# Kernel tuning notes

Measured on AMD Instinct MI355X. Metric: run time of the kernel, lower is better.

## Reference

```python
import jax, jax.numpy as jnp
import numpy as np

N = 50000
E = 600000
IN_DIM = 2000
HID = 64
OUT_DIM = 25
HEADS = 4
NHEAD = 4
NLAYERS = 2
FF = 2048
EPS = 1e-5


def gat_conv(x, W, a_src, a_dst, b, src, dst, heads, out_dim):
    n = x.shape[0]
    h = (x @ W).reshape(n, heads, out_dim)
    # per-node attention logits
    al_src = jnp.sum(h * a_src[None], axis=-1)  # [N,H]
    al_dst = jnp.sum(h * a_dst[None], axis=-1)  # [N,H]
    e = jax.nn.leaky_relu(al_src[src] + al_dst[dst], negative_slope=0.2)  # [E,H]
    # segment softmax over destination nodes (every node has a self-loop)
    m = jax.ops.segment_max(e, dst, num_segments=n)
    ex = jnp.exp(e - m[dst])
    s = jax.ops.segment_sum(ex, dst, num_segments=n)
    alpha = ex / (s[dst] + 1e-16)  # [E,H]
    msg = h[src] * alpha[..., None]  # [E,H,out]
    out = jax.ops.segment_sum(msg, dst, num_segments=n)  # [N,H,out]
    return out.reshape(n, heads * out_dim) + b


def layer_norm(x, g, b):
    mu = jnp.mean(x, axis=-1, keepdims=True)
    var = jnp.mean(jnp.square(x - mu), axis=-1, keepdims=True)
    return (x - mu) * jax.lax.rsqrt(var + EPS) * g + b


def encoder_layer(x, Wq, Wk, Wv, bq, bk, bv, Wo, bo, g1, b1, Wf1, bf1, Wf2, bf2, g2, b2):
    # seq_len = 1: each node is its own length-1 sequence -> softmax weights are 1
    n, d = x.shape
    dh = d // NHEAD
    q = (x @ Wq + bq).reshape(n, NHEAD, dh)
    k = (x @ Wk + bk).reshape(n, NHEAD, dh)
    v = (x @ Wv + bv).reshape(n, NHEAD, dh)
    s = jnp.sum(q * k, axis=-1, keepdims=True) / jnp.sqrt(jnp.float32(dh))  # [N,H,1]
    a = jax.nn.softmax(s, axis=-1)  # all ones (length-1 softmax)
    attn = (a * v).reshape(n, d) @ Wo + bo
    x = layer_norm(x + attn, g1, b1)
    ff = jax.nn.relu(x @ Wf1 + bf1) @ Wf2 + bf2
    return layer_norm(x + ff, g2, b2)


def setup_inputs() -> dict:
    key = jax.random.key(0)
    ks = jax.random.split(key, 40)
    sc = 0.05
    inp = {}
    inp["x"] = jax.random.normal(ks[0], (N, IN_DIM), dtype=jnp.float32)
    inp["edge_src"] = jax.random.randint(ks[1], (E,), 0, N, dtype=jnp.int32)
    inp["edge_dst"] = jax.random.randint(ks[2], (E,), 0, N, dtype=jnp.int32)
    # GAT layer 1: in -> hidden, heads=4
    inp["W1"] = jax.random.normal(ks[3], (IN_DIM, HEADS * HID), dtype=jnp.float32) * sc
    inp["a_src1"] = jax.random.normal(ks[4], (HEADS, HID), dtype=jnp.float32) * sc
    inp["a_dst1"] = jax.random.normal(ks[5], (HEADS, HID), dtype=jnp.float32) * sc
    inp["b1"] = jnp.zeros((HEADS * HID,), dtype=jnp.float32)
    # GAT layer 2: hidden*heads -> hidden, heads=1
    inp["W2"] = jax.random.normal(ks[6], (HEADS * HID, HID), dtype=jnp.float32) * sc
    inp["a_src2"] = jax.random.normal(ks[7], (1, HID), dtype=jnp.float32) * sc
    inp["a_dst2"] = jax.random.normal(ks[8], (1, HID), dtype=jnp.float32) * sc
    inp["b2"] = jnp.zeros((HID,), dtype=jnp.float32)
    # Transformer fusion params, stacked over layers
    def pl(k, shape):
        return jax.random.normal(k, shape, dtype=jnp.float32) * sc
    inp["t_Wq"] = pl(ks[9], (NLAYERS, HID, HID))
    inp["t_Wk"] = pl(ks[10], (NLAYERS, HID, HID))
    inp["t_Wv"] = pl(ks[11], (NLAYERS, HID, HID))
    inp["t_bq"] = jnp.zeros((NLAYERS, HID), dtype=jnp.float32)
    inp["t_bk"] = jnp.zeros((NLAYERS, HID), dtype=jnp.float32)
    inp["t_bv"] = jnp.zeros((NLAYERS, HID), dtype=jnp.float32)
    inp["t_Wo"] = pl(ks[12], (NLAYERS, HID, HID))
    inp["t_bo"] = jnp.zeros((NLAYERS, HID), dtype=jnp.float32)
    inp["t_ln1g"] = jnp.ones((NLAYERS, HID), dtype=jnp.float32)
    inp["t_ln1b"] = jnp.zeros((NLAYERS, HID), dtype=jnp.float32)
    inp["t_Wff1"] = pl(ks[13], (NLAYERS, HID, FF))
    inp["t_bff1"] = jnp.zeros((NLAYERS, FF), dtype=jnp.float32)
    inp["t_Wff2"] = pl(ks[14], (NLAYERS, FF, HID))
    inp["t_bff2"] = jnp.zeros((NLAYERS, HID), dtype=jnp.float32)
    inp["t_ln2g"] = jnp.ones((NLAYERS, HID), dtype=jnp.float32)
    inp["t_ln2b"] = jnp.zeros((NLAYERS, HID), dtype=jnp.float32)
    # GAT ADT head: hidden -> out, heads=1
    inp["W3"] = pl(ks[15], (HID, OUT_DIM))
    inp["a_src3"] = pl(ks[16], (1, OUT_DIM))
    inp["a_dst3"] = pl(ks[17], (1, OUT_DIM))
    inp["b3"] = jnp.zeros((OUT_DIM,), dtype=jnp.float32)
    return inp


def reference(x, edge_src, edge_dst, W1, a_src1, a_dst1, b1, W2, a_src2, a_dst2, b2,
              t_Wq, t_Wk, t_Wv, t_bq, t_bk, t_bv, t_Wo, t_bo, t_ln1g, t_ln1b,
              t_Wff1, t_bff1, t_Wff2, t_bff2, t_ln2g, t_ln2b,
              W3, a_src3, a_dst3, b3):
    # add self-loops (PyG GATConv default add_self_loops=True)
    loops = jnp.arange(N, dtype=edge_src.dtype)
    src = jnp.concatenate([edge_src, loops])
    dst = jnp.concatenate([edge_dst, loops])

    h = gat_conv(x, W1, a_src1, a_dst1, b1, src, dst, HEADS, HID)
    h = jax.nn.elu(h)
    rna = gat_conv(h, W2, a_src2, a_dst2, b2, src, dst, 1, HID)
    rna = jax.nn.elu(rna)

    fused = rna
    for l in range(NLAYERS):
        fused = encoder_layer(fused, t_Wq[l], t_Wk[l], t_Wv[l], t_bq[l], t_bk[l], t_bv[l],
                              t_Wo[l], t_bo[l], t_ln1g[l], t_ln1b[l],
                              t_Wff1[l], t_bff1[l], t_Wff2[l], t_bff2[l],
                              t_ln2g[l], t_ln2b[l])

    adt_pred = gat_conv(fused, W3, a_src3, a_dst3, b3, src, dst, 1, OUT_DIM)
    return (adt_pred, fused)
```

## Files before the change

kernel.cpp:

```cpp
#include <hip/hip_runtime.h>
#include <math.h>

#define N_NODES 50000
#define IN_DIMC 2000
#define FF_DIM 2048
#define EPSV 1e-5f
#define SCAN_B 1024

typedef __attribute__((ext_vector_type(8))) short sh8;
typedef __attribute__((ext_vector_type(4))) short sh4;
typedef __attribute__((ext_vector_type(4))) float f32x4;

__device__ __forceinline__ void splitf(float f, unsigned short& h, unsigned short& l) {
    unsigned u = __float_as_uint(f);
    h = (unsigned short)(u >> 16);
    float fh = __uint_as_float(u & 0xFFFF0000u);
    l = (unsigned short)(__float_as_uint(f - fh) >> 16);
}

__device__ __forceinline__ void split8(f32x4 a0, f32x4 a1, sh8& hh, sh8& ll) {
    float f[8] = {a0[0], a0[1], a0[2], a0[3], a1[0], a1[1], a1[2], a1[3]};
    sh8 h, l;
#pragma unroll
    for (int j = 0; j < 8; j++) {
        unsigned u = __float_as_uint(f[j]);
        h[j] = (short)(u >> 16);
        float fhi = __uint_as_float(u & 0xFFFF0000u);
        l[j] = (short)(__float_as_uint(f[j] - fhi) >> 16);
    }
    hh = h; ll = l;
}

__device__ __forceinline__ void gload_lds16(const float* g, float* l) {
    __builtin_amdgcn_global_load_lds(
        (const __attribute__((address_space(1))) unsigned int*)g,
        (__attribute__((address_space(3))) unsigned int*)l, 16, 0, 0);
}

__global__ void k_zero_i32(int* p, int n) {
    int i = blockIdx.x * blockDim.x + threadIdx.x;
    if (i < n) p[i] = 0;
}

__global__ void k_hist(const int* __restrict__ dst, int* __restrict__ deg, int E, int n) {
    int i = blockIdx.x * blockDim.x + threadIdx.x;
    if (i < E + n) {
        int d = (i < E) ? dst[i] : (i - E);
        atomicAdd(&deg[d], 1);
    }
}

__global__ __launch_bounds__(1024) void k_scan1(const int* __restrict__ deg, int* __restrict__ rstart,
                                                int* __restrict__ part, int n) {
    __shared__ int lds[SCAN_B];
    int t = threadIdx.x;
    int base = blockIdx.x * SCAN_B;
    int v = (base + t < n) ? deg[base + t] : 0;
    lds[t] = v;
    __syncthreads();
    for (int o = 1; o < SCAN_B; o <<= 1) {
        int add = (t >= o) ? lds[t - o] : 0;
        __syncthreads();
        lds[t] += add;
        __syncthreads();
    }
    if (base + t < n) rstart[base + t] = lds[t] - v;
    if (t == SCAN_B - 1) part[blockIdx.x] = lds[t];
}

__global__ void k_scan2(int* part, int nb) {
    if (threadIdx.x == 0 && blockIdx.x == 0) {
        int s = 0;
        for (int i = 0; i < nb; i++) { int v = part[i]; part[i] = s; s += v; }
    }
}

__global__ void k_scan3(int* rstart, const int* __restrict__ part, int n) {
    int i = blockIdx.x * blockDim.x + threadIdx.x;
    if (i < n) rstart[i] += part[i / SCAN_B];
}

__global__ void k_scatter(const int* __restrict__ src, const int* __restrict__ dst,
                          const int* __restrict__ rstart, int* __restrict__ cursor,
                          int* __restrict__ csr_src, int E, int n) {
    int i = blockIdx.x * blockDim.x + threadIdx.x;
    if (i < E + n) {
        int s, d;
        if (i < E) { s = src[i]; d = dst[i]; } else { s = i - E; d = s; }
        int pos = rstart[d] + atomicAdd(&cursor[d], 1);
        csr_src[pos] = s;
    }
}

__global__ void k_wsplit_pad(const float* __restrict__ W, short* __restrict__ oh,
                             short* __restrict__ ol, int K, int N, int Kpad, int Npad) {
    int i = blockIdx.x * blockDim.x + threadIdx.x;
    if (i < Kpad * Npad) {
        int c = i / Kpad, k = i - c * Kpad;
        float v = (c < N && k < K) ? W[(size_t)k * N + c] : 0.f;
        unsigned short h, l;
        splitf(v, h, l);
        oh[i] = (short)h; ol[i] = (short)l;
    }
}

__global__ void k_wsplit(const float* __restrict__ W, short* __restrict__ oh,
                         short* __restrict__ ol, int K, int N) {
    int i = blockIdx.x * blockDim.x + threadIdx.x;
    if (i < K * N) {
        int k = i / N, c = i - k * N;
        unsigned short h, l;
        splitf(W[i], h, l);
        oh[(size_t)c * K + k] = (short)h;
        ol[(size_t)c * K + k] = (short)l;
    }
}

__global__ void k_wcomb(const float* __restrict__ Wv, const float* __restrict__ bv,
                        const float* __restrict__ Wo, const float* __restrict__ bo,
                        short* __restrict__ och, short* __restrict__ ocl, float* __restrict__ bc) {
    int i = blockIdx.x * blockDim.x + threadIdx.x;
    if (i < 4096) {
        int cc = i & 63, kk = i >> 6;
        float s = 0.f;
        for (int j = 0; j < 64; j++) s += Wv[kk * 64 + j] * Wo[j * 64 + cc];
        unsigned short h, l;
        splitf(s, h, l);
        och[cc * 64 + kk] = (short)h;
        ocl[cc * 64 + kk] = (short)l;
        if (kk == 0) {
            float t = bo[cc];
            for (int j = 0; j < 64; j++) t += bv[j] * Wo[j * 64 + cc];
            bc[cc] = t;
        }
    }
}

template<int NF>
__global__ __launch_bounds__(256, 2) void k_gemm_x(const float* __restrict__ A,
                                                   const short* __restrict__ Bth,
                                                   const short* __restrict__ Btl,
                                                   const float* __restrict__ bias,
                                                   float* __restrict__ C,
                                                   int M, int N, int K, int Kpad) {
    constexpr int BN = NF * 32;
    __shared__ float Afs[128 * 64];
    __shared__ short Bhs[BN * 64];
    __shared__ short Bls[BN * 64];
    int tid = threadIdx.x;
    int wave = tid >> 6, lane = tid & 63;
    int wm = wave & 1, wn = wave >> 1;
    int l15 = lane & 15, l4 = lane >> 4;
    long m0 = (long)blockIdx.x * 128;
    int n0 = blockIdx.y * BN;
    int chunks = K >> 2;
    int cmax = chunks - 1;
    int ktiles = (chunks + 15) >> 4;
    f32x4 acc[4][NF] = {};
    int Sl = wave * 512 + lane;
    for (int kt = 0; kt < ktiles; kt++) {
        int c0 = kt << 4;
#pragma unroll
        for (int i = 0; i < 8; i++) {
            int S = Sl + i * 64;
            int row = S >> 4, slot = S & 15;
            long srcrow = m0 + row; if (srcrow > (long)M - 1) srcrow = M - 1;
            int ch = c0 + (slot ^ (row & 7)); if (ch > cmax) ch = cmax;
            gload_lds16(A + (size_t)srcrow * K + (size_t)ch * 4,
                        &Afs[(wave * 512 + i * 64) * 4]);
        }
#pragma unroll
        for (int p = 0; p < NF; p++) {
            int u = tid + p * 256;
            int col = u >> 3, k8 = u & 7;
            size_t src = (size_t)(n0 + col) * Kpad + (size_t)kt * 64 + k8 * 8;
            sh8 bh = *(const sh8*)&Bth[src];
            sh8 bl = *(const sh8*)&Btl[src];
            int doff = col * 64 + ((k8 ^ (col & 7)) << 3);
            *(sh8*)&Bhs[doff] = bh;
            *(sh8*)&Bls[doff] = bl;
        }
        __syncthreads();
#pragma unroll
        for (int kf = 0; kf < 2; kf++) {
            sh8 ah[4], al[4];
#pragma unroll
            for (int mf = 0; mf < 4; mf++) {
                int row = wm * 64 + mf * 16 + l15;
                int s0 = kf * 8 + l4 * 2;
                f32x4 a0 = *(const f32x4*)&Afs[row * 64 + ((s0 ^ (row & 7)) << 2)];
                f32x4 a1 = *(const f32x4*)&Afs[row * 64 + (((s0 + 1) ^ (row & 7)) << 2)];
                split8(a0, a1, ah[mf], al[mf]);
            }
#pragma unroll
            for (int nf = 0; nf < NF; nf++) {
                int col = wn * (NF * 16) + nf * 16 + l15;
                int k8 = kf * 4 + l4;
                int boff = col * 64 + ((k8 ^ (col & 7)) << 3);
                sh8 bh = *(const sh8*)&Bhs[boff];
                sh8 bl = *(const sh8*)&Bls[boff];
#pragma unroll
                for (int mf = 0; mf < 4; mf++) {
                    f32x4 c = acc[mf][nf];
                    c = __builtin_amdgcn_mfma_f32_16x16x32_bf16(ah[mf], bh, c, 0, 0, 0);
                    c = __builtin_amdgcn_mfma_f32_16x16x32_bf16(ah[mf], bl, c, 0, 0, 0);
                    c = __builtin_amdgcn_mfma_f32_16x16x32_bf16(al[mf], bh, c, 0, 0, 0);
                    acc[mf][nf] = c;
                }
            }
        }
        __syncthreads();
    }
#pragma unroll
    for (int mf = 0; mf < 4; mf++)
#pragma unroll
        for (int r = 0; r < 4; r++) {
            long gm = m0 + wm * 64 + mf * 16 + l4 * 4 + r;
            if (gm >= M) continue;
#pragma unroll
            for (int nf = 0; nf < NF; nf++) {
                int gc = n0 + wn * (NF * 16) + nf * 16 + l15;
                if (gc < N) C[gm * (size_t)N + gc] = acc[mf][nf][r] + (bias ? bias[gc] : 0.f);
            }
        }
}

__global__ __launch_bounds__(256, 2) void k_ff_mfma(const float* __restrict__ x,
                                                    const short* __restrict__ W1h, const short* __restrict__ W1l,
                                                    const float* __restrict__ bf1,
                                                    const short* __restrict__ W2h, const short* __restrict__ W2l,
                                                    const float* __restrict__ bf2,
                                                    float* __restrict__ out, int n) {
    __shared__ short lds[36864];
    short* Hh = lds;
    short* Hl = lds + 9216;
    short* w1h = lds + 18432;
    short* w1l = lds + 23040;
    short* w2h = lds + 27648;
    short* w2l = lds + 32256;
    int tid = threadIdx.x;
    int wave = tid >> 6, lane = tid & 63;
    int wm = wave & 1, wn = wave >> 1;
    int l15 = lane & 15, l4 = lane >> 4;
    long row0 = (long)blockIdx.x * 128;
#pragma unroll
    for (int p = 0; p < 8; p++) {
        int f4 = tid + p * 256;
        int row = f4 >> 4, kq = f4 & 15;
        long gr = row0 + row;
        float4 a = {0.f, 0.f, 0.f, 0.f};
        if (gr < n) a = *(const float4*)&x[gr * 64 + kq * 4];
        unsigned short h0, h1, h2, h3, l0, l1, l2, l3;
        splitf(a.x, h0, l0); splitf(a.y, h1, l1);
        splitf(a.z, h2, l2); splitf(a.w, h3, l3);
        sh4 hv = {(short)h0, (short)h1, (short)h2, (short)h3};
        sh4 lv = {(short)l0, (short)l1, (short)l2, (short)l3};
        *(sh4*)&Hh[row * 72 + kq * 4] = hv;
        *(sh4*)&Hl[row * 72 + kq * 4] = lv;
    }
    __syncthreads();
    sh8 xh[4][2], xl[4][2];
#pragma unroll
    for (int mf = 0; mf < 4; mf++)
#pragma unroll
        for (int kf = 0; kf < 2; kf++) {
            int off = (wm * 64 + mf * 16 + l15) * 72 + kf * 32 + l4 * 8;
            xh[mf][kf] = *(const sh8*)&Hh[off];
            xl[mf][kf] = *(const sh8*)&Hl[off];
        }
    f32x4 acc2[4][2] = {};
    for (int j0 = 0; j0 < FF_DIM; j0 += 64) {
#pragma unroll
        for (int p = 0; p < 2; p++) {
            int u = tid + p * 256;
            int cj = u >> 3, kq8 = u & 7;
            *(sh8*)&w1h[cj * 72 + kq8 * 8] = *(const sh8*)&W1h[(size_t)(j0 + cj) * 64 + kq8 * 8];
            *(sh8*)&w1l[cj * 72 + kq8 * 8] = *(const sh8*)&W1l[(size_t)(j0 + cj) * 64 + kq8 * 8];
            *(sh8*)&w2h[cj * 72 + kq8 * 8] = *(const sh8*)&W2h[(size_t)cj * FF_DIM + j0 + kq8 * 8];
            *(sh8*)&w2l[cj * 72 + kq8 * 8] = *(const sh8*)&W2l[(size_t)cj * FF_DIM + j0 + kq8 * 8];
        }
        __syncthreads();
        f32x4 hacc[4][2] = {};
#pragma unroll
        for (int kf = 0; kf < 2; kf++) {
            sh8 bh[2], bl[2];
#pragma unroll
            for (int nf = 0; nf < 2; nf++) {
                int off = (wn * 32 + nf * 16 + l15) * 72 + kf * 32 + l4 * 8;
                bh[nf] = *(const sh8*)&w1h[off];
                bl[nf] = *(const sh8*)&w1l[off];
            }
#pragma unroll
            for (int mf = 0; mf < 4; mf++)
#pragma unroll
                for (int nf = 0; nf < 2; nf++) {
                    f32x4 c = hacc[mf][nf];
                    c = __builtin_amdgcn_mfma_f32_16x16x32_bf16(xh[mf][kf], bh[nf], c, 0, 0, 0);
                    c = __builtin_amdgcn_mfma_f32_16x16x32_bf16(xh[mf][kf], bl[nf], c, 0, 0, 0);
                    c = __builtin_amdgcn_mfma_f32_16x16x32_bf16(xl[mf][kf], bh[nf], c, 0, 0, 0);
                    hacc[mf][nf] = c;
                }
        }
#pragma unroll
        for (int mf = 0; mf < 4; mf++)
#pragma unroll
            for (int nf = 0; nf < 2; nf++) {
                int col = wn * 32 + nf * 16 + l15;
                float b1v = bf1[j0 + col];
#pragma unroll
                for (int r = 0; r < 4; r++) {
                    int row = wm * 64 + mf * 16 + l4 * 4 + r;
                    float v = fmaxf(hacc[mf][nf][r] + b1v, 0.f);
                    unsigned short h, l;
                    splitf(v, h, l);
                    Hh[row * 72 + col] = (short)h;
                    Hl[row * 72 + col] = (short)l;
                }
            }
        __syncthreads();
#pragma unroll
        for (int kf = 0; kf < 2; kf++) {
            sh8 ah[4], alv[4], bh[2], bl[2];
#pragma unroll
            for (int mf = 0; mf < 4; mf++) {
                int off = (wm * 64 + mf * 16 + l15) * 72 + kf * 32 + l4 * 8;
                ah[mf] = *(const sh8*)&Hh[off];
                alv[mf] = *(const sh8*)&Hl[off];
            }
#pragma unroll
            for (int nf = 0; nf < 2; nf++) {
                int off = (wn * 32 + nf * 16 + l15) * 72 + kf * 32 + l4 * 8;
                bh[nf] = *(const sh8*)&w2h[off];
                bl[nf] = *(const sh8*)&w2l[off];
            }
#pragma unroll
            for (int mf = 0; mf < 4; mf++)
#pragma unroll
                for (int nf = 0; nf < 2; nf++) {
                    f32x4 c = acc2[mf][nf];
                    c = __builtin_amdgcn_mfma_f32_16x16x32_bf16(ah[mf], bh[nf], c, 0, 0, 0);
                    c = __builtin_amdgcn_mfma_f32_16x16x32_bf16(ah[mf], bl[nf], c, 0, 0, 0);
                    c = __builtin_amdgcn_mfma_f32_16x16x32_bf16(alv[mf], bh[nf], c, 0, 0, 0);
                    acc2[mf][nf] = c;
                }
        }
        __syncthreads();
    }
#pragma unroll
    for (int mf = 0; mf < 4; mf++)
#pragma unroll
        for (int r = 0; r < 4; r++) {
            long gr = row0 + wm * 64 + mf * 16 + l4 * 4 + r;
            if (gr >= n) continue;
#pragma unroll
            for (int nf = 0; nf < 2; nf++) {
                int gc = wn * 32 + nf * 16 + l15;
                out[gr * 64 + gc] = acc2[mf][nf][r] + bf2[gc];
            }
        }
}

template<int H, int D>
__global__ void k_al(const float* __restrict__ h, const float* __restrict__ a_src,
                     const float* __restrict__ a_dst, float* __restrict__ als,
                     float* __restrict__ ald, int n) {
    long w = ((long)blockIdx.x * blockDim.x + threadIdx.x) >> 6;
    int lane = threadIdx.x & 63;
    long nn = w / H;
    int hh = (int)(w % H);
    if (nn >= n) return;
    float v = 0.f, u = 0.f;
    if (lane < D) {
        float hv = h[nn * (H * D) + hh * D + lane];
        v = hv * a_src[hh * D + lane];
        u = hv * a_dst[hh * D + lane];
    }
#pragma unroll
    for (int o = 32; o > 0; o >>= 1) {
        v += __shfl_xor(v, o, 64);
        u += __shfl_xor(u, o, 64);
    }
    if (lane == 0) { als[nn * H + hh] = v; ald[nn * H + hh] = u; }
}

template<int H, int D, bool DO_ELU>
__global__ __launch_bounds__(256) void k_gat_agg_w(const float* __restrict__ h,
                                                   const float* __restrict__ als,
                                                   const float* __restrict__ ald,
                                                   const float* __restrict__ bias,
                                                   const int* __restrict__ rstart,
                                                   const int* __restrict__ deg,
                                                   const int* __restrict__ csr_src,
                                                   float* __restrict__ out, int n) {
    int wid = (int)(((long)blockIdx.x * blockDim.x + threadIdx.x) >> 6);
    int lane = threadIdx.x & 63;
    if (wid >= n) return;
    int beg = rstart[wid], cnt = deg[wid];
    float aldv = 0.f;
    if (lane < H) aldv = ald[wid * H + lane];
    float wsum = 0.f;
    float acc[H];
#pragma unroll
    for (int i = 0; i < H; i++) acc[i] = 0.f;
    for (int e = 0; e < cnt; e++) {
        int s = csr_src[beg + e];
        float w = 0.f;
        if (lane < H) {
            float lg = als[s * H + lane] + aldv;
            lg = (lg > 0.f) ? lg : 0.2f * lg;
            w = __expf(lg);
            wsum += w;
        }
#pragma unroll
        for (int hh = 0; hh < H; hh++) {
            float wv = __shfl(w, hh, 64);
            float hv = (lane < D) ? h[(size_t)s * (H * D) + hh * D + lane] : 0.f;
            acc[hh] += wv * hv;
        }
    }
#pragma unroll
    for (int hh = 0; hh < H; hh++) {
        float ws = __shfl(wsum, hh, 64);
        if (lane < D) {
            float v = acc[hh] / (ws + 1e-16f) + bias[hh * D + lane];
            if (DO_ELU) v = (v > 0.f) ? v : expm1f(v);
            out[(size_t)wid * (H * D) + hh * D + lane] = v;
        }
    }
}

__global__ void k_ln(const float* __restrict__ x, const float* __restrict__ y,
                     const float* __restrict__ g, const float* __restrict__ b,
                     float* __restrict__ out, int n) {
    long w = ((long)blockIdx.x * blockDim.x + threadIdx.x) >> 6;
    int lane = threadIdx.x & 63;
    if (w >= n) return;
    float v = x[w * 64 + lane] + y[w * 64 + lane];
    float s = v;
#pragma unroll
    for (int o = 32; o > 0; o >>= 1) s += __shfl_xor(s, o, 64);
    float mu = s * (1.f / 64.f);
    float dv = v - mu;
    float q = dv * dv;
#pragma unroll
    for (int o = 32; o > 0; o >>= 1) q += __shfl_xor(q, o, 64);
    float var = q * (1.f / 64.f);
    out[w * 64 + lane] = dv * rsqrtf(var + EPSV) * g[lane] + b[lane];
}

extern "C" void kernel_launch(void* const* d_in, const int* in_sizes, int n_in,
                              void* d_out, int out_size, void* d_ws, size_t ws_size,
                              hipStream_t stream) {
    const float* x = (const float*)d_in[0];
    const int* esrc = (const int*)d_in[1];
    const int* edst = (const int*)d_in[2];
    const float* W1 = (const float*)d_in[3];
    const float* as1 = (const float*)d_in[4];
    const float* ad1 = (const float*)d_in[5];
    const float* b1 = (const float*)d_in[6];
    const float* W2 = (const float*)d_in[7];
    const float* as2 = (const float*)d_in[8];
    const float* ad2 = (const float*)d_in[9];
    const float* b2 = (const float*)d_in[10];
    const float* tWv = (const float*)d_in[13];
    const float* tbv = (const float*)d_in[16];
    const float* tWo = (const float*)d_in[17];
    const float* tbo = (const float*)d_in[18];
    const float* tg1 = (const float*)d_in[19];
    const float* tb1 = (const float*)d_in[20];
    const float* tWf1 = (const float*)d_in[21];
    const float* tbf1 = (const float*)d_in[22];
    const float* tWf2 = (const float*)d_in[23];
    const float* tbf2 = (const float*)d_in[24];
    const float* tg2 = (const float*)d_in[25];
    const float* tb2 = (const float*)d_in[26];
    const float* W3 = (const float*)d_in[27];
    const float* as3 = (const float*)d_in[28];
    const float* ad3 = (const float*)d_in[29];
    const float* b3 = (const float*)d_in[30];

    const int n = N_NODES;
    const int E = in_sizes[1];
    const int ET = E + n;

    float* fw = (float*)d_ws;
    float* h1 = fw;
    float* agg1 = fw + 12800000;
    float* bufA = fw + 25600000;
    float* bufB = fw + 28800000;
    float* bufC = fw + 32000000;
    float* bufD = fw + 35200000;
    float* als = fw + 38400000;
    float* ald = fw + 38600000;
    float* bc = fw + 38800000;
    int* deg = (int*)(fw + 38800064);
    int* rstart = deg + 50016;
    int* cursor = rstart + 50016;
    int* part = cursor + 50016;
    int* csr = part + 64;
    short* sbase = (short*)(csr + 700000);
    short* w1th = sbase;
    short* w1tl = w1th + 524288;
    short* w2th = w1tl + 524288;
    short* w2tl = w2th + 16384;
    short* w3th = w2tl + 16384;
    short* w3tl = w3th + 4096;
    short* wcth = w3tl + 4096;
    short* wctl = wcth + 4096;
    const size_t WFS = 131072;
    short* wf1h = wctl + 4096;
    short* wf1l = wf1h + 2 * WFS;
    short* wf2h = wf1l + 2 * WFS;
    short* wf2l = wf2h + 2 * WFS;
    float* h3 = h1;

    float* outAdt = (float*)d_out;
    float* outFused = outAdt + (size_t)n * 25;

    k_zero_i32<<<(150048 + 255) / 256, 256, 0, stream>>>(deg, 150048);
    k_hist<<<(ET + 255) / 256, 256, 0, stream>>>(edst, deg, E, n);
    int nsb = (n + SCAN_B - 1) / SCAN_B;
    k_scan1<<<nsb, SCAN_B, 0, stream>>>(deg, rstart, part, n);
    k_scan2<<<1, 64, 0, stream>>>(part, nsb);
    k_scan3<<<(n + 255) / 256, 256, 0, stream>>>(rstart, part, n);
    k_scatter<<<(ET + 255) / 256, 256, 0, stream>>>(esrc, edst, rstart, cursor, csr, E, n);

    k_wsplit_pad<<<(524288 + 255) / 256, 256, 0, stream>>>(W1, w1th, w1tl, IN_DIMC, 256, 2048, 256);
    k_wsplit_pad<<<(16384 + 255) / 256, 256, 0, stream>>>(W2, w2th, w2tl, 256, 64, 256, 64);
    k_wsplit_pad<<<(4096 + 255) / 256, 256, 0, stream>>>(W3, w3th, w3tl, 64, 25, 64, 64);
    for (int l = 0; l < 2; l++) {
        k_wsplit<<<(131072 + 255) / 256, 256, 0, stream>>>(tWf1 + (size_t)l * 64 * FF_DIM,
                                                           wf1h + l * WFS, wf1l + l * WFS, 64, FF_DIM);
        k_wsplit<<<(131072 + 255) / 256, 256, 0, stream>>>(tWf2 + (size_t)l * FF_DIM * 64,
                                                           wf2h + l * WFS, wf2l + l * WFS, FF_DIM, 64);
    }

    k_gemm_x<4><<<dim3((n + 127) / 128, 2), 256, 0, stream>>>(x, w1th, w1tl, nullptr, h1, n, 256, IN_DIMC, 2048);
    k_al<4, 64><<<n, 256, 0, stream>>>(h1, as1, ad1, als, ald, n);
    k_gat_agg_w<4, 64, true><<<(n + 3) / 4, 256, 0, stream>>>(h1, als, ald, b1, rstart, deg, csr, agg1, n);

    k_gemm_x<2><<<dim3((n + 127) / 128, 1), 256, 0, stream>>>(agg1, w2th, w2tl, nullptr, bufA, n, 64, 256, 256);
    k_al<1, 64><<<(n + 3) / 4, 256, 0, stream>>>(bufA, as2, ad2, als, ald, n);
    k_gat_agg_w<1, 64, true><<<(n + 3) / 4, 256, 0, stream>>>(bufA, als, ald, b2, rstart, deg, csr, bufB, n);

    float* xin = bufB;
    for (int l = 0; l < 2; l++) {
        k_wcomb<<<16, 256, 0, stream>>>(tWv + (size_t)l * 4096, tbv + (size_t)l * 64,
                                        tWo + (size_t)l * 4096, tbo + (size_t)l * 64,
                                        wcth, wctl, bc);
        k_gemm_x<2><<<dim3((n + 127) / 128, 1), 256, 0, stream>>>(xin, wcth, wctl, bc, bufD, n, 64, 64, 64);
        k_ln<<<(n + 3) / 4, 256, 0, stream>>>(xin, bufD, tg1 + (size_t)l * 64, tb1 + (size_t)l * 64, bufA, n);
        k_ff_mfma<<<(n + 127) / 128, 256, 0, stream>>>(bufA, wf1h + l * WFS, wf1l + l * WFS,
                                                       tbf1 + (size_t)l * FF_DIM,
                                                       wf2h + l * WFS, wf2l + l * WFS,
                                                       tbf2 + (size_t)l * 64, bufC, n);
        float* xout = (l == 1) ? outFused : bufB;
        k_ln<<<(n + 3) / 4, 256, 0, stream>>>(bufA, bufC, tg2 + (size_t)l * 64, tb2 + (size_t)l * 64, xout, n);
        xin = xout;
    }

    k_gemm_x<2><<<dim3((n + 127) / 128, 1), 256, 0, stream>>>(outFused, w3th, w3tl, nullptr, h3, n, 25, 64, 64);
    k_al<1, 25><<<(n + 3) / 4, 256, 0, stream>>>(h3, as3, ad3, als, ald, n);
    k_gat_agg_w<1, 25, false><<<(n + 3) / 4, 256, 0, stream>>>(h3, als, ald, b3, rstart, deg, csr, outAdt, n);
}
```

Measured before the change: 1.484 ms.

## Double-buffer GEMM tiles via direct LDS loads and vectorize GAT aggregation kernels

The split-bf16 GEMM now uses two LDS buffers with a K-tile of 32, and loads B high/low halves directly into LDS with global_load_lds, so the next tile is fetched while MFMAs run on the current one. The generic GAT aggregation kernel is replaced by three specialized ones. The 4-head version uses float4 loads and processes two edges per iteration. The single-head versions split the wave across several edges at once and reduce with shuffles. The aim is to hide load latency in the large first GEMM and to cut idle lanes and scalar gathers in the bandwidth-bound edge aggregation. The cost is more synchronization per K step and extra register pressure.

```diff
diff --git a/kernel.cpp b/kernel.cpp
--- a/kernel.cpp
+++ b/kernel.cpp
@@ -31,7 +31,7 @@
     hh = h; ll = l;
 }
 
-__device__ __forceinline__ void gload_lds16(const float* g, float* l) {
+__device__ __forceinline__ void gload_lds16(const void* g, void* l) {
     __builtin_amdgcn_global_load_lds(
         (const __attribute__((address_space(1))) unsigned int*)g,
         (__attribute__((address_space(3))) unsigned int*)l, 16, 0, 0);
@@ -137,79 +137,80 @@
 }
 
 template<int NF>
-__global__ __launch_bounds__(256, 2) void k_gemm_x(const float* __restrict__ A,
+__global__ __launch_bounds__(256, 2) void k_gemm_p(const float* __restrict__ A,
                                                    const short* __restrict__ Bth,
                                                    const short* __restrict__ Btl,
                                                    const float* __restrict__ bias,
                                                    float* __restrict__ C,
                                                    int M, int N, int K, int Kpad) {
     constexpr int BN = NF * 32;
-    __shared__ float Afs[128 * 64];
-    __shared__ short Bhs[BN * 64];
-    __shared__ short Bls[BN * 64];
+    constexpr int NB = BN / 32;
+    __shared__ float Afs[2][128 * 32];
+    __shared__ short Bs[2][BN * 64];
     int tid = threadIdx.x;
     int wave = tid >> 6, lane = tid & 63;
     int wm = wave & 1, wn = wave >> 1;
     int l15 = lane & 15, l4 = lane >> 4;
     long m0 = (long)blockIdx.x * 128;
     int n0 = blockIdx.y * BN;
-    int chunks = K >> 2;
-    int cmax = chunks - 1;
-    int ktiles = (chunks + 15) >> 4;
+    int cmax = (K >> 2) - 1;
+    int ktiles = (K + 31) >> 5;
     f32x4 acc[4][NF] = {};
-    int Sl = wave * 512 + lane;
-    for (int kt = 0; kt < ktiles; kt++) {
-        int c0 = kt << 4;
-#pragma unroll
-        for (int i = 0; i < 8; i++) {
-            int S = Sl + i * 64;
-            int row = S >> 4, slot = S & 15;
+
+    auto stage = [&](int kt, int b) {
+        int c0 = kt << 3;
+#pragma unroll
+        for (int i = 0; i < 4; i++) {
+            int S = (wave * 4 + i) * 64 + lane;
+            int row = S >> 3, slot = S & 7;
             long srcrow = m0 + row; if (srcrow > (long)M - 1) srcrow = M - 1;
             int ch = c0 + (slot ^ (row & 7)); if (ch > cmax) ch = cmax;
             gload_lds16(A + (size_t)srcrow * K + (size_t)ch * 4,
-                        &Afs[(wave * 512 + i * 64) * 4]);
-        }
-#pragma unroll
-        for (int p = 0; p < NF; p++) {
-            int u = tid + p * 256;
-            int col = u >> 3, k8 = u & 7;
-            size_t src = (size_t)(n0 + col) * Kpad + (size_t)kt * 64 + k8 * 8;
-            sh8 bh = *(const sh8*)&Bth[src];
-            sh8 bl = *(const sh8*)&Btl[src];
-            int doff = col * 64 + ((k8 ^ (col & 7)) << 3);
-            *(sh8*)&Bhs[doff] = bh;
-            *(sh8*)&Bls[doff] = bl;
+                        &Afs[b][(wave * 4 + i) * 256]);
+        }
+#pragma unroll
+        for (int i = 0; i < NB; i++) {
+            int S = (wave * NB + i) * 64 + lane;
+            int col = S >> 3, slot = S & 7;
+            int c = slot ^ (col & 7);
+            const short* src = (c < 4)
+                ? Bth + (size_t)(n0 + col) * Kpad + kt * 32 + c * 8
+                : Btl + (size_t)(n0 + col) * Kpad + kt * 32 + (c - 4) * 8;
+            gload_lds16(src, &Bs[b][(wave * NB + i) * 512]);
+        }
+    };
+
+    stage(0, 0);
+    __syncthreads();
+    int b = 0;
+    for (int kt = 0; kt < ktiles; kt++) {
+        if (kt + 1 < ktiles) stage(kt + 1, b ^ 1);
+        sh8 ah[4], al[4];
+#pragma unroll
+        for (int mf = 0; mf < 4; mf++) {
+            int row = wm * 64 + mf * 16 + l15;
+            int s0 = l4 * 2;
+            f32x4 a0 = *(const f32x4*)&Afs[b][row * 32 + ((s0 ^ (row & 7)) << 2)];
+            f32x4 a1 = *(const f32x4*)&Afs[b][row * 32 + (((s0 + 1) ^ (row & 7)) << 2)];
+            split8(a0, a1, ah[mf], al[mf]);
+        }
+#pragma unroll
+        for (int nf = 0; nf < NF; nf++) {
+            int col = wn * (NF * 16) + nf * 16 + l15;
+            int sh = l4 ^ (col & 7);
+            sh8 bh = *(const sh8*)&Bs[b][col * 64 + (sh << 3)];
+            sh8 bl = *(const sh8*)&Bs[b][col * 64 + ((sh ^ 4) << 3)];
+#pragma unroll
+            for (int mf = 0; mf < 4; mf++) {
+                f32x4 c = acc[mf][nf];
+                c = __builtin_amdgcn_mfma_f32_16x16x32_bf16(ah[mf], bh, c, 0, 0, 0);
+                c = __builtin_amdgcn_mfma_f32_16x16x32_bf16(ah[mf], bl, c, 0, 0, 0);
+                c = __builtin_amdgcn_mfma_f32_16x16x32_bf16(al[mf], bh, c, 0, 0, 0);
+                acc[mf][nf] = c;
+            }
         }
         __syncthreads();
-#pragma unroll
-        for (int kf = 0; kf < 2; kf++) {
-            sh8 ah[4], al[4];
-#pragma unroll
-            for (int mf = 0; mf < 4; mf++) {
-                int row = wm * 64 + mf * 16 + l15;
-                int s0 = kf * 8 + l4 * 2;
-                f32x4 a0 = *(const f32x4*)&Afs[row * 64 + ((s0 ^ (row & 7)) << 2)];
-                f32x4 a1 = *(const f32x4*)&Afs[row * 64 + (((s0 + 1) ^ (row & 7)) << 2)];
-                split8(a0, a1, ah[mf], al[mf]);
-            }
-#pragma unroll
-            for (int nf = 0; nf < NF; nf++) {
-                int col = wn * (NF * 16) + nf * 16 + l15;
-                int k8 = kf * 4 + l4;
-                int boff = col * 64 + ((k8 ^ (col & 7)) << 3);
-                sh8 bh = *(const sh8*)&Bhs[boff];
-                sh8 bl = *(const sh8*)&Bls[boff];
-#pragma unroll
-                for (int mf = 0; mf < 4; mf++) {
-                    f32x4 c = acc[mf][nf];
-                    c = __builtin_amdgcn_mfma_f32_16x16x32_bf16(ah[mf], bh, c, 0, 0, 0);
-                    c = __builtin_amdgcn_mfma_f32_16x16x32_bf16(ah[mf], bl, c, 0, 0, 0);
-                    c = __builtin_amdgcn_mfma_f32_16x16x32_bf16(al[mf], bh, c, 0, 0, 0);
-                    acc[mf][nf] = c;
-                }
-            }
-        }
-        __syncthreads();
+        b ^= 1;
     }
 #pragma unroll
     for (int mf = 0; mf < 4; mf++)
@@ -383,50 +384,146 @@
     if (lane == 0) { als[nn * H + hh] = v; ald[nn * H + hh] = u; }
 }
 
-template<int H, int D, bool DO_ELU>
-__global__ __launch_bounds__(256) void k_gat_agg_w(const float* __restrict__ h,
-                                                   const float* __restrict__ als,
-                                                   const float* __restrict__ ald,
-                                                   const float* __restrict__ bias,
-                                                   const int* __restrict__ rstart,
-                                                   const int* __restrict__ deg,
-                                                   const int* __restrict__ csr_src,
-                                                   float* __restrict__ out, int n) {
+template<bool DO_ELU>
+__global__ __launch_bounds__(256) void k_agg4(const float* __restrict__ h,
+                                              const float* __restrict__ als,
+                                              const float* __restrict__ ald,
+                                              const float* __restrict__ bias,
+                                              const int* __restrict__ rstart,
+                                              const int* __restrict__ deg,
+                                              const int* __restrict__ csr,
+                                              float* __restrict__ out, int n) {
     int wid = (int)(((long)blockIdx.x * blockDim.x + threadIdx.x) >> 6);
     int lane = threadIdx.x & 63;
     if (wid >= n) return;
     int beg = rstart[wid], cnt = deg[wid];
-    float aldv = 0.f;
-    if (lane < H) aldv = ald[wid * H + lane];
+    int hh = lane >> 4;
+    float aldv = (lane < 4) ? ald[wid * 4 + lane] : 0.f;
+    const float4* h4 = (const float4*)h;
+    float4 acc = {0.f, 0.f, 0.f, 0.f};
     float wsum = 0.f;
-    float acc[H];
-#pragma unroll
-    for (int i = 0; i < H; i++) acc[i] = 0.f;
-    for (int e = 0; e < cnt; e++) {
-        int s = csr_src[beg + e];
-        float w = 0.f;
-        if (lane < H) {
-            float lg = als[s * H + lane] + aldv;
+    for (int e = 0; e < cnt; e += 2) {
+        bool has1 = (e + 1 < cnt);
+        int s0 = csr[beg + e];
+        int s1 = csr[beg + (has1 ? e + 1 : e)];
+        float4 h0 = h4[(size_t)s0 * 64 + lane];
+        float4 h1 = h4[(size_t)s1 * 64 + lane];
+        float w0 = 0.f, w1 = 0.f;
+        if (lane < 4) {
+            float lg = als[s0 * 4 + lane] + aldv;
             lg = (lg > 0.f) ? lg : 0.2f * lg;
-            w = __expf(lg);
-            wsum += w;
-        }
-#pragma unroll
-        for (int hh = 0; hh < H; hh++) {
-            float wv = __shfl(w, hh, 64);
-            float hv = (lane < D) ? h[(size_t)s * (H * D) + hh * D + lane] : 0.f;
-            acc[hh] += wv * hv;
-        }
-    }
-#pragma unroll
-    for (int hh = 0; hh < H; hh++) {
-        float ws = __shfl(wsum, hh, 64);
-        if (lane < D) {
-            float v = acc[hh] / (ws + 1e-16f) + bias[hh * D + lane];
-            if (DO_ELU) v = (v > 0.f) ? v : expm1f(v);
-            out[(size_t)wid * (H * D) + hh * D + lane] = v;
-        }
-    }
+            w0 = __expf(lg);
+            if (has1) {
+                float lg1 = als[s1 * 4 + lane] + aldv;
+                lg1 = (lg1 > 0.f) ? lg1 : 0.2f * lg1;
+                w1 = __expf(lg1);
+            }
+            wsum += w0 + w1;
+        }
+        float w0b = __shfl(w0, hh, 64);
+        float w1b = __shfl(w1, hh, 64);
+        acc.x += w0b * h0.x + w1b * h1.x;
+        acc.y += w0b * h0.y + w1b * h1.y;
+        acc.z += w0b * h0.z + w1b * h1.z;
+        acc.w += w0b * h0.w + w1b * h1.w;
+    }
+    float ws = __shfl(wsum, hh, 64) + 1e-16f;
+    float4 bv = *(const float4*)&bias[lane * 4];
+    float4 o;
+    o.x = acc.x / ws + bv.x; o.y = acc.y / ws + bv.y;
+    o.z = acc.z / ws + bv.z; o.w = acc.w / ws + bv.w;
+    if (DO_ELU) {
+        o.x = (o.x > 0.f) ? o.x : expm1f(o.x);
+        o.y = (o.y > 0.f) ? o.y : expm1f(o.y);
+        o.z = (o.z > 0.f) ? o.z : expm1f(o.z);
+        o.w = (o.w > 0.f) ? o.w : expm1f(o.w);
+    }
+    *(float4*)&out[(size_t)wid * 256 + lane * 4] = o;
+}
+
+template<bool DO_ELU>
+__global__ __launch_bounds__(256) void k_agg1_64(const float* __restrict__ h,
+                                                 const float* __restrict__ als,
+                                                 const float* __restrict__ ald,
+                                                 const float* __restrict__ bias,
+                                                 const int* __restrict__ rstart,
+                                                 const int* __restrict__ deg,
+                                                 const int* __restrict__ csr,
+                                                 float* __restrict__ out, int n) {
+    int wid = (int)(((long)blockIdx.x * blockDim.x + threadIdx.x) >> 6);
+    int lane = threadIdx.x & 63;
+    if (wid >= n) return;
+    int beg = rstart[wid], cnt = deg[wid];
+    int g = lane >> 4, el = lane & 15;
+    float aldv = ald[wid];
+    const float4* h4 = (const float4*)h;
+    float4 acc = {0.f, 0.f, 0.f, 0.f};
+    float sw = 0.f;
+    for (int e = 0; e < cnt; e += 4) {
+        int eg = e + g;
+        bool act = eg < cnt;
+        int s = csr[beg + (act ? eg : cnt - 1)];
+        float4 hv = h4[(size_t)s * 16 + el];
+        float lg = als[s] + aldv;
+        lg = (lg > 0.f) ? lg : 0.2f * lg;
+        float w = act ? __expf(lg) : 0.f;
+        sw += w;
+        acc.x += w * hv.x; acc.y += w * hv.y;
+        acc.z += w * hv.z; acc.w += w * hv.w;
+    }
+#pragma unroll
+    for (int o = 16; o < 64; o <<= 1) {
+        sw += __shfl_xor(sw, o, 64);
+        acc.x += __shfl_xor(acc.x, o, 64);
+        acc.y += __shfl_xor(acc.y, o, 64);
+        acc.z += __shfl_xor(acc.z, o, 64);
+        acc.w += __shfl_xor(acc.w, o, 64);
+    }
+    if (lane < 16) {
+        float ws = sw + 1e-16f;
+        float4 bv = *(const float4*)&bias[lane * 4];
+        float4 o;
+        o.x = acc.x / ws + bv.x; o.y = acc.y / ws + bv.y;
+        o.z = acc.z / ws + bv.z; o.w = acc.w / ws + bv.w;
+        if (DO_ELU) {
+            o.x = (o.x > 0.f) ? o.x : expm1f(o.x);
+            o.y = (o.y > 0.f) ? o.y : expm1f(o.y);
+            o.z = (o.z > 0.f) ? o.z : expm1f(o.z);
+            o.w = (o.w > 0.f) ? o.w : expm1f(o.w);
+        }
+        *(float4*)&out[(size_t)wid * 64 + lane * 4] = o;
+    }
+}
+
+__global__ __launch_bounds__(256) void k_agg1_25(const float* __restrict__ h,
+                                                 const float* __restrict__ als,
+                                                 const float* __restrict__ ald,
+                                                 const float* __restrict__ bias,
+                                                 const int* __restrict__ rstart,
+                                                 const int* __restrict__ deg,
+                                                 const int* __restrict__ csr,
+                                                 float* __restrict__ out, int n) {
+    int wid = (int)(((long)blockIdx.x * blockDim.x + threadIdx.x) >> 6);
+    int lane = threadIdx.x & 63;
+    if (wid >= n) return;
+    int beg = rstart[wid], cnt = deg[wid];
+    int g = lane >> 5, el = lane & 31;
+    float aldv = ald[wid];
+    float acc = 0.f, sw = 0.f;
+    for (int e = 0; e < cnt; e += 2) {
+        int eg = e + g;
+        bool act = eg < cnt;
+        int s = csr[beg + (act ? eg : cnt - 1)];
+        float hv = (el < 25) ? h[(size_t)s * 25 + el] : 0.f;
+        float lg = als[s] + aldv;
+        lg = (lg > 0.f) ? lg : 0.2f * lg;
+        float w = act ? __expf(lg) : 0.f;
+        sw += w;
+        acc += w * hv;
+    }
+    sw += __shfl_xor(sw, 32, 64);
+    acc += __shfl_xor(acc, 32, 64);
+    if (lane < 25) out[(size_t)wid * 25 + lane] = acc / (sw + 1e-16f) + bias[lane];
 }
 
 __global__ void k_ln(const float* __restrict__ x, const float* __restrict__ y,
@@ -535,20 +632,20 @@
                                                            wf2h + l * WFS, wf2l + l * WFS, FF_DIM, 64);
     }
 
-    k_gemm_x<4><<<dim3((n + 127) / 128, 2), 256, 0, stream>>>(x, w1th, w1tl, nullptr, h1, n, 256, IN_DIMC, 2048);
+    k_gemm_p<4><<<dim3((n + 127) / 128, 2), 256, 0, stream>>>(x, w1th, w1tl, nullptr, h1, n, 256, IN_DIMC, 2048);
     k_al<4, 64><<<n, 256, 0, stream>>>(h1, as1, ad1, als, ald, n);
-    k_gat_agg_w<4, 64, true><<<(n + 3) / 4, 256, 0, stream>>>(h1, als, ald, b1, rstart, deg, csr, agg1, n);
-
-    k_gemm_x<2><<<dim3((n + 127) / 128, 1), 256, 0, stream>>>(agg1, w2th, w2tl, nullptr, bufA, n, 64, 256, 256);
+    k_agg4<true><<<(n + 3) / 4, 256, 0, stream>>>(h1, als, ald, b1, rstart, deg, csr, agg1, n);
+
+    k_gemm_p<2><<<dim3((n + 127) / 128, 1), 256, 0, stream>>>(agg1, w2th, w2tl, nullptr, bufA, n, 64, 256, 256);
     k_al<1, 64><<<(n + 3) / 4, 256, 0, stream>>>(bufA, as2, ad2, als, ald, n);
-    k_gat_agg_w<1, 64, true><<<(n + 3) / 4, 256, 0, stream>>>(bufA, als, ald, b2, rstart, deg, csr, bufB, n);
+    k_agg1_64<true><<<(n + 3) / 4, 256, 0, stream>>>(bufA, als, ald, b2, rstart, deg, csr, bufB, n);
 
     float* xin = bufB;
     for (int l = 0; l < 2; l++) {
         k_wcomb<<<16, 256, 0, stream>>>(tWv + (size_t)l * 4096, tbv + (size_t)l * 64,
                                         tWo + (size_t)l * 4096, tbo + (size_t)l * 64,
                                         wcth, wctl, bc);
-        k_gemm_x<2><<<dim3((n + 127) / 128, 1), 256, 0, stream>>>(xin, wcth, wctl, bc, bufD, n, 64, 64, 64);
+        k_gemm_p<2><<<dim3((n + 127) / 128, 1), 256, 0, stream>>>(xin, wcth, wctl, bc, bufD, n, 64, 64, 64);
         k_ln<<<(n + 3) / 4, 256, 0, stream>>>(xin, bufD, tg1 + (size_t)l * 64, tb1 + (size_t)l * 64, bufA, n);
         k_ff_mfma<<<(n + 127) / 128, 256, 0, stream>>>(bufA, wf1h + l * WFS, wf1l + l * WFS,
                                                        tbf1 + (size_t)l * FF_DIM,
@@ -559,7 +656,7 @@
         xin = xout;
     }
 
-    k_gemm_x<2><<<dim3((n + 127) / 128, 1), 256, 0, stream>>>(outFused, w3th, w3tl, nullptr, h3, n, 25, 64, 64);
+    k_gemm_p<2><<<dim3((n + 127) / 128, 1), 256, 0, stream>>>(outFused, w3th, w3tl, nullptr, h3, n, 25, 64, 64);
     k_al<1, 25><<<(n + 3) / 4, 256, 0, stream>>>(h3, as3, ad3, als, ald, n);
-    k_gat_agg_w<1, 25, false><<<(n + 3) / 4, 256, 0, stream>>>(h3, als, ald, b3, rstart, deg, csr, outAdt, n);
-}
+    k_agg1_25<<<(n + 3) / 4, 256, 0, stream>>>(h3, als, ald, b3, rstart, deg, csr, outAdt, n);
+}
```

Result: faster. 1.394 ms (-6.1%).
